# Performance work log

Hardware: AMD Instinct MI355X
Metric: run time of the kernel (lower is better)

## Reference

```python
import jax, jax.numpy as jnp
import numpy as np

B = 16      # number of point clouds
N = 4096    # points per cloud (max after densify)
D = 3       # xyz


def setup_inputs() -> dict:
    key = jax.random.key(0)
    k1, k2 = jax.random.split(key)
    pred = jax.random.normal(k1, (B * N, D), dtype=jnp.float32)
    target = jax.random.normal(k2, (B * N, D), dtype=jnp.float32)
    # sorted segment ids, equal-sized clouds (faithful to to_dense_batch usage)
    batch = jnp.repeat(jnp.arange(B, dtype=jnp.int64), N)
    return {"pred": pred, "target": target, "batch": batch}


def to_dense_batch(x, batch, num_batches, max_n):
    # PyG to_dense_batch: scatter flat points into [B, max_n, D], zero-padded.
    ones = jnp.ones_like(batch)
    counts = jax.ops.segment_sum(ones, batch, num_segments=num_batches)
    offsets = jnp.concatenate([jnp.zeros((1,), batch.dtype), jnp.cumsum(counts)[:-1]])
    pos = jnp.arange(batch.shape[0], dtype=batch.dtype) - offsets[batch]
    dense = jnp.zeros((num_batches, max_n, x.shape[-1]), x.dtype)
    return dense.at[batch, pos].set(x)


def chamfer_distance(x, y):
    # squared-euclidean pairwise distances via the GEMM identity
    x2 = jnp.sum(x * x, axis=-1)                      # [B, N]
    y2 = jnp.sum(y * y, axis=-1)                      # [B, M]
    xy = jnp.einsum('bnd,bmd->bnm', x, y)             # [B, N, M]
    d = x2[:, :, None] + y2[:, None, :] - 2.0 * xy    # [B, N, M]
    cham_x = jnp.mean(jnp.min(d, axis=2), axis=1)     # mean over N of min over M
    cham_y = jnp.mean(jnp.min(d, axis=1), axis=1)     # mean over M of min over N
    # point_reduction='mean', batch_reduction='mean' (pytorch3d defaults)
    return jnp.mean(cham_x + cham_y)


def reference(pred, target, batch):
    x = to_dense_batch(pred, batch, B, N)
    y = to_dense_batch(target, batch, B, N)
    return chamfer_distance(x, y)
```

## Files before the change

kernel.cpp:

```cpp
#include <hip/hip_runtime.h>


namespace {

constexpr int kB = 16;
constexpr int kN = 4096;
constexpr int kPlane = kB * kN;
constexpr int kJS = 4;
constexpr int kStage = 256;
constexpr int kNS = (kN / kJS) / kStage;
constexpr float kScale = 1.0f / (float)(kB * kN);

typedef short bf16x8 __attribute__((ext_vector_type(8)));
typedef float f32x4 __attribute__((ext_vector_type(4)));
typedef unsigned short u16;

__device__ inline u16 bf16_rn(float f) {
  union { float f; unsigned u; } v; v.f = f;
  unsigned r = v.u + 0x7fffu + ((v.u >> 16) & 1u);
  return (u16)(r >> 16);
}
__device__ inline float bf16_f(u16 h) {
  union { unsigned u; float f; } v; v.u = (unsigned)h << 16;
  return v.f;
}
__device__ inline unsigned pk2(u16 lo, u16 hi) {
  return (unsigned)lo | ((unsigned)hi << 16);
}

__global__ void init_out(float* out) { out[0] = 0.0f; }

__global__ __launch_bounds__(256) void cd_prep(
    const float* __restrict__ pred, const float* __restrict__ targ,
    u16* __restrict__ Apred, u16* __restrict__ Atarg,
    u16* __restrict__ Bpred, u16* __restrict__ Btarg,
    float* __restrict__ out) {
  const int p = blockIdx.x * 256 + threadIdx.x;
  if (p == 0) out[0] = 0.0f;
  const int cloud = p >> 12, q = p & (kN - 1);
  const int stg = q >> 8, pl = q & (kStage - 1);
  const size_t boff = (size_t)cloud * 65536 + (size_t)stg * 4096 + (size_t)pl * 8;
  const u16 one = 0x3F80;

  const float* srcs[2] = {pred, targ};
  u16* adsts[2] = {Apred, Atarg};
  u16* bdsts[2] = {Bpred, Btarg};
#pragma unroll
  for (int which = 0; which < 2; ++which) {
    const float a = srcs[which][3 * p], c = srcs[which][3 * p + 1],
                d = srcs[which][3 * p + 2];
    const u16 ah = bf16_rn(a), ch = bf16_rn(c), dh = bf16_rn(d);
    const u16 al = bf16_rn(a - bf16_f(ah));
    const u16 cl = bf16_rn(c - bf16_f(ch));
    const u16 dl = bf16_rn(d - bf16_f(dh));
    const float s2 = fmaf(a, a, fmaf(c, c, d * d));
    const u16 s2h = bf16_rn(s2);
    const u16 s2l = bf16_rn(s2 - bf16_f(s2h));
    {
      uint4 w0, w1;
      w0.x = pk2(ah, ch); w0.y = pk2(dh, al); w0.z = pk2(cl, dl); w0.w = pk2(ah, ch);
      w1.x = pk2(dh, al); w1.y = pk2(cl, dl); w1.z = pk2(s2h, s2l); w1.w = pk2(one, one);
      uint4* dst = reinterpret_cast<uint4*>(adsts[which] + (size_t)p * 16);
      dst[0] = w0; dst[1] = w1;
    }
    {
      const u16 nah = bf16_rn(-2.0f * bf16_f(ah));
      const u16 nch = bf16_rn(-2.0f * bf16_f(ch));
      const u16 ndh = bf16_rn(-2.0f * bf16_f(dh));
      const u16 nal = bf16_rn(-2.0f * bf16_f(al));
      const u16 ncl = bf16_rn(-2.0f * bf16_f(cl));
      const u16 ndl = bf16_rn(-2.0f * bf16_f(dl));
      uint4 w0, w1;
      w0.x = pk2(nah, nch); w0.y = pk2(ndh, nah); w0.z = pk2(nch, ndh); w0.w = pk2(nal, ncl);
      w1.x = pk2(ndl, nal); w1.y = pk2(ncl, ndl); w1.z = pk2(one, one); w1.w = pk2(s2h, s2l);
      *reinterpret_cast<uint4*>(bdsts[which] + boff) = w0;
      *reinterpret_cast<uint4*>(bdsts[which] + boff + 2048) = w1;
    }
  }
}

__global__ __launch_bounds__(256) void cd_mfma(
    const u16* __restrict__ Apred, const u16* __restrict__ Atarg,
    const u16* __restrict__ Bpred, const u16* __restrict__ Btarg,
    float* __restrict__ rowpart) {
  __shared__ uint4 Blds4[1028];

  const int t = threadIdx.x;
  const int w = t >> 6, lane = t & 63;
  const int l15 = lane & 15, kg = lane >> 4;
  const bool act = (kg < 2);
  const int g = kg & 1;
  const int bx = blockIdx.x;
  const int chunk = bx & 31;
  const int slice = bx >> 5;
  const int cloud = blockIdx.y;
  const int dir = blockIdx.z;
  const u16* __restrict__ A = dir ? Atarg : Apred;
  const u16* __restrict__ B = dir ? Bpred : Btarg;

  const int arow0 = cloud * kN + chunk * 128 + w * 32 + l15;
  union { uint4 u; bf16x8 v; } af0, af1;
  af0.u = make_uint4(0, 0, 0, 0);
  af1.u = make_uint4(0, 0, 0, 0);
  if (act) {
    af0.u = *reinterpret_cast<const uint4*>(A + (size_t)arow0 * 16 + g * 8);
    af1.u = *reinterpret_cast<const uint4*>(A + (size_t)(arow0 + 16) * 16 + g * 8);
  }

  const char* bsl = (const char*)B + (size_t)cloud * 131072 + (size_t)slice * 32768;
  char* ldsbase = (char*)Blds4;
#define STAGE(st, buf)                                                        \
  {                                                                           \
    const char* _src = bsl + (size_t)(st) * 8192;                             \
    char* _dst = ldsbase + (buf) * 8192;                                      \
    _Pragma("unroll")                                                         \
    for (int i = 0; i < 2; ++i) {                                             \
      __builtin_amdgcn_global_load_lds(                                       \
          (const __attribute__((address_space(1))) void*)(_src +              \
              ((w * 2 + i) * 64 + lane) * 16),                                \
          (__attribute__((address_space(3))) void*)(_dst + (w * 2 + i) * 1024),\
          16, 0, 0);                                                          \
    }                                                                         \
  }

  const int rb0 = act ? (g * 4096 + l15 * 16) : 16384;
  const int rstep = act ? 256 : 0;
  const int bufstep = act ? 8192 : 0;

  f32x4 z4;
#pragma unroll
  for (int r = 0; r < 4; ++r) z4[r] = 0.0f;
  float rmin0[4], rmin1[4];
#pragma unroll
  for (int r = 0; r < 4; ++r) { rmin0[r] = 1e30f; rmin1[r] = 1e30f; }

  STAGE(0, 0);
  if (t == 0) Blds4[1024] = make_uint4(0, 0, 0, 0);
  __syncthreads();

  for (int st = 0; st < kNS; ++st) {
    if (st < kNS - 1) STAGE(st + 1, (st + 1) & 1);
    const char* pb = ldsbase + rb0 + (st & 1) * bufstep;
#pragma unroll 4
    for (int jt = 0; jt < kStage / 16; ++jt) {
      union { uint4 u; bf16x8 v; } bu;
      bu.u = *reinterpret_cast<const uint4*>(pb);
      pb += rstep;
      const f32x4 s0 =
          __builtin_amdgcn_mfma_f32_16x16x32_bf16(af0.v, bu.v, z4, 0, 0, 0);
      const f32x4 s1 =
          __builtin_amdgcn_mfma_f32_16x16x32_bf16(af1.v, bu.v, z4, 0, 0, 0);
#pragma unroll
      for (int r = 0; r < 4; ++r) {
        rmin0[r] = fminf(rmin0[r], s0[r]);
        rmin1[r] = fminf(rmin1[r], s1[r]);
      }
    }
    __syncthreads();
  }
#undef STAGE

#pragma unroll
  for (int sh = 1; sh < 16; sh <<= 1) {
#pragma unroll
    for (int r = 0; r < 4; ++r) {
      rmin0[r] = fminf(rmin0[r], __shfl_xor(rmin0[r], sh, 64));
      rmin1[r] = fminf(rmin1[r], __shfl_xor(rmin1[r], sh, 64));
    }
  }
  if (l15 == 0) {
    float* rp = rowpart + (((size_t)dir * kJS + slice) * kB + cloud) * kN +
                chunk * 128 + w * 32;
#pragma unroll
    for (int r = 0; r < 4; ++r) {
      rp[kg * 4 + r] = rmin0[r];
      rp[16 + kg * 4 + r] = rmin1[r];
    }
  }
}

__global__ __launch_bounds__(256) void cd_reduce(
    const float* __restrict__ rowpart, float* __restrict__ out) {
  const int u = blockIdx.x * 256 + threadIdx.x;
  const int dir = u >> 16, rest = u & 65535;
  const int cloud = rest >> 12, row = rest & (kN - 1);
  float rm = 1e30f;
#pragma unroll
  for (int s2 = 0; s2 < kJS; ++s2)
    rm = fminf(rm, rowpart[(((size_t)dir * kJS + s2) * kB + cloud) * kN + row]);
  float s = rm;
  for (int o = 32; o > 0; o >>= 1) s += __shfl_down(s, o, 64);
  __shared__ float wsum[4];
  const int lane = threadIdx.x & 63, wv = threadIdx.x >> 6;
  if (lane == 0) wsum[wv] = s;
  __syncthreads();
  if (threadIdx.x == 0)
    atomicAdd(out, (wsum[0] + wsum[1] + wsum[2] + wsum[3]) * kScale);
}

template <int KX>
__global__ __launch_bounds__(256) void chamfer_direct(
    const float* __restrict__ pred, const float* __restrict__ targ,
    float* __restrict__ out) {
  __shared__ float4 tA[128], tB[128];
  const int t = threadIdx.x;
  const int xb = blockIdx.x, b = blockIdx.y, dir = blockIdx.z;
  const float* __restrict__ X = dir ? targ : pred;
  const float* __restrict__ Y = dir ? pred : targ;
  float2 xx2[KX], xy2[KX], xz2[KX];
  float x2[KX], mn[KX];
  const int ibase = b * kN + xb * (256 * KX) + t;
#pragma unroll
  for (int k = 0; k < KX; ++k) {
    const int i = ibase + k * 256;
    const float a = X[3 * i], c = X[3 * i + 1], d = X[3 * i + 2];
    x2[k] = fmaf(a, a, fmaf(c, c, d * d));
    xx2[k] = make_float2(-2.0f * a, -2.0f * a);
    xy2[k] = make_float2(-2.0f * c, -2.0f * c);
    xz2[k] = make_float2(-2.0f * d, -2.0f * d);
    mn[k] = 1e30f;
  }
  for (int t0 = 0; t0 < kN; t0 += 256) {
    __syncthreads();
    if (t < 128) {
      const int j0 = 3 * (b * kN + t0 + 2 * t);
      const float a0 = Y[j0], c0 = Y[j0 + 1], d0 = Y[j0 + 2];
      const float a1 = Y[j0 + 3], c1 = Y[j0 + 4], d1 = Y[j0 + 5];
      tA[t] = make_float4(a0, a1, c0, c1);
      tB[t] = make_float4(d0, d1, fmaf(a0, a0, fmaf(c0, c0, d0 * d0)),
                          fmaf(a1, a1, fmaf(c1, c1, d1 * d1)));
    }
    __syncthreads();
    for (int jj = 0; jj < 128; ++jj) {
      const float4 qa = tA[jj], qb = tB[jj];
      const float2 qx = make_float2(qa.x, qa.y), qy = make_float2(qa.z, qa.w);
      const float2 qz = make_float2(qb.x, qb.y), qw = make_float2(qb.z, qb.w);
#pragma unroll
      for (int k = 0; k < KX; ++k) {
        float2 acc;
        asm("v_pk_fma_f32 %0, %1, %2, %3\n\t"
            "v_pk_fma_f32 %0, %4, %5, %0\n\t"
            "v_pk_fma_f32 %0, %6, %7, %0"
            : "=&v"(acc)
            : "v"(xz2[k]), "v"(qz), "v"(qw), "v"(xy2[k]), "v"(qy),
              "v"(xx2[k]), "v"(qx));
        asm("v_min3_f32 %0, %0, %1, %2" : "+v"(mn[k]) : "v"(acc.x), "v"(acc.y));
      }
    }
  }
  float s = 0.0f;
#pragma unroll
  for (int k = 0; k < KX; ++k) s += x2[k] + mn[k];
  for (int o = 32; o > 0; o >>= 1) s += __shfl_down(s, o, 64);
  __shared__ float wsum[4];
  const int lane = t & 63, wv = t >> 6;
  if (lane == 0) wsum[wv] = s;
  __syncthreads();
  if (t == 0)
    atomicAdd(out, (wsum[0] + wsum[1] + wsum[2] + wsum[3]) * kScale);
}

}

extern "C" void kernel_launch(void* const* d_in, const int* in_sizes, int n_in,
                              void* d_out, int out_size, void* d_ws,
                              size_t ws_size, hipStream_t stream) {
  const float* pred = (const float*)d_in[0];
  const float* targ = (const float*)d_in[1];
  float* out = (float*)d_out;

  const size_t needOne = (size_t)kPlane * 16 * sizeof(u16);
  const size_t needRow = (size_t)2 * kJS * kPlane * sizeof(float) / kB * kB;
  const size_t needRowB = (size_t)2 * kJS * kB * kN * sizeof(float);
  (void)needRow;
  if (ws_size >= 4 * needOne + needRowB) {
    u16* Apred = (u16*)d_ws;
    u16* Atarg = (u16*)((char*)d_ws + needOne);
    u16* Bpred = (u16*)((char*)d_ws + 2 * needOne);
    u16* Btarg = (u16*)((char*)d_ws + 3 * needOne);
    float* rowpart = (float*)((char*)d_ws + 4 * needOne);
    cd_prep<<<dim3(kPlane / 256), 256, 0, stream>>>(pred, targ, Apred, Atarg,
                                                    Bpred, Btarg, out);
    cd_mfma<<<dim3(32 * kJS, kB, 2), 256, 0, stream>>>(Apred, Atarg, Bpred,
                                                       Btarg, rowpart);
    cd_reduce<<<dim3(2 * kPlane / 256), 256, 0, stream>>>(rowpart, out);
  } else {
    init_out<<<dim3(1), dim3(1), 0, stream>>>(out);
    constexpr int KX = 8;
    dim3 grid(kN / (256 * KX), kB, 2);
    chamfer_direct<KX><<<grid, 256, 0, stream>>>(pred, targ, out);
  }
}
```

Measured before the change: 106.4 us.

## Switch distance MFMA to 32x32x16 bf16 with min3 reduction and fewer slices

Replaces the 16x16x32 MFMA tiles, where half the lanes were idle and fed zero operands, with 32x32x16 MFMA tiles that use all 64 lanes. The A/B packed layouts are reordered to match the new K-split across lane halves. Per-row minima are folded with v_min3 across two MFMA results, and the column-slice count drops from 4 to 2, so each block handles more columns and the reduce pass reads fewer partials. The costs are a larger accumulator register footprint per wave and half as many blocks, which lowers parallelism.

```diff
diff --git a/kernel.cpp b/kernel.cpp
--- a/kernel.cpp
+++ b/kernel.cpp
@@ -6,13 +6,13 @@
 constexpr int kB = 16;
 constexpr int kN = 4096;
 constexpr int kPlane = kB * kN;
-constexpr int kJS = 4;
+constexpr int kJS = 2;
 constexpr int kStage = 256;
 constexpr int kNS = (kN / kJS) / kStage;
 constexpr float kScale = 1.0f / (float)(kB * kN);
 
 typedef short bf16x8 __attribute__((ext_vector_type(8)));
-typedef float f32x4 __attribute__((ext_vector_type(4)));
+typedef float f32x16 __attribute__((ext_vector_type(16)));
 typedef unsigned short u16;
 
 __device__ inline u16 bf16_rn(float f) {
@@ -59,7 +59,7 @@
     {
       uint4 w0, w1;
       w0.x = pk2(ah, ch); w0.y = pk2(dh, al); w0.z = pk2(cl, dl); w0.w = pk2(ah, ch);
-      w1.x = pk2(dh, al); w1.y = pk2(cl, dl); w1.z = pk2(s2h, s2l); w1.w = pk2(one, one);
+      w1.x = pk2(dh, s2h); w1.y = pk2(s2l, one); w1.z = pk2(one, al); w1.w = pk2(cl, dl);
       uint4* dst = reinterpret_cast<uint4*>(adsts[which] + (size_t)p * 16);
       dst[0] = w0; dst[1] = w1;
     }
@@ -72,7 +72,7 @@
       const u16 ndl = bf16_rn(-2.0f * bf16_f(dl));
       uint4 w0, w1;
       w0.x = pk2(nah, nch); w0.y = pk2(ndh, nah); w0.z = pk2(nch, ndh); w0.w = pk2(nal, ncl);
-      w1.x = pk2(ndl, nal); w1.y = pk2(ncl, ndl); w1.z = pk2(one, one); w1.w = pk2(s2h, s2l);
+      w1.x = pk2(ndl, one); w1.y = pk2(one, s2h); w1.z = pk2(s2l, nal); w1.w = pk2(ncl, ndl);
       *reinterpret_cast<uint4*>(bdsts[which] + boff) = w0;
       *reinterpret_cast<uint4*>(bdsts[which] + boff + 2048) = w1;
     }
@@ -83,13 +83,11 @@
     const u16* __restrict__ Apred, const u16* __restrict__ Atarg,
     const u16* __restrict__ Bpred, const u16* __restrict__ Btarg,
     float* __restrict__ rowpart) {
-  __shared__ uint4 Blds4[1028];
+  __shared__ uint4 Blds4[1024];
 
   const int t = threadIdx.x;
   const int w = t >> 6, lane = t & 63;
-  const int l15 = lane & 15, kg = lane >> 4;
-  const bool act = (kg < 2);
-  const int g = kg & 1;
+  const int half = lane >> 5, l31 = lane & 31;
   const int bx = blockIdx.x;
   const int chunk = bx & 31;
   const int slice = bx >> 5;
@@ -98,16 +96,13 @@
   const u16* __restrict__ A = dir ? Atarg : Apred;
   const u16* __restrict__ B = dir ? Bpred : Btarg;
 
-  const int arow0 = cloud * kN + chunk * 128 + w * 32 + l15;
-  union { uint4 u; bf16x8 v; } af0, af1;
-  af0.u = make_uint4(0, 0, 0, 0);
-  af1.u = make_uint4(0, 0, 0, 0);
-  if (act) {
-    af0.u = *reinterpret_cast<const uint4*>(A + (size_t)arow0 * 16 + g * 8);
-    af1.u = *reinterpret_cast<const uint4*>(A + (size_t)(arow0 + 16) * 16 + g * 8);
-  }
-
-  const char* bsl = (const char*)B + (size_t)cloud * 131072 + (size_t)slice * 32768;
+  const int arow = cloud * kN + chunk * 128 + w * 32 + l31;
+  union U { uint4 u; bf16x8 v; };
+  U af;
+  af.u = *reinterpret_cast<const uint4*>(A + (size_t)arow * 16 + half * 8);
+
+  const char* bsl = (const char*)B + (size_t)cloud * 131072 +
+                    (size_t)slice * 65536;
   char* ldsbase = (char*)Blds4;
 #define STAGE(st, buf)                                                        \
   {                                                                           \
@@ -123,58 +118,50 @@
     }                                                                         \
   }
 
-  const int rb0 = act ? (g * 4096 + l15 * 16) : 16384;
-  const int rstep = act ? 256 : 0;
-  const int bufstep = act ? 8192 : 0;
-
-  f32x4 z4;
-#pragma unroll
-  for (int r = 0; r < 4; ++r) z4[r] = 0.0f;
-  float rmin0[4], rmin1[4];
-#pragma unroll
-  for (int r = 0; r < 4; ++r) { rmin0[r] = 1e30f; rmin1[r] = 1e30f; }
+  f32x16 zacc;
+#pragma unroll
+  for (int r = 0; r < 16; ++r) zacc[r] = 0.0f;
+  float rmin[16];
+#pragma unroll
+  for (int r = 0; r < 16; ++r) rmin[r] = 1e30f;
 
   STAGE(0, 0);
-  if (t == 0) Blds4[1024] = make_uint4(0, 0, 0, 0);
   __syncthreads();
 
   for (int st = 0; st < kNS; ++st) {
     if (st < kNS - 1) STAGE(st + 1, (st + 1) & 1);
-    const char* pb = ldsbase + rb0 + (st & 1) * bufstep;
-#pragma unroll 4
-    for (int jt = 0; jt < kStage / 16; ++jt) {
-      union { uint4 u; bf16x8 v; } bu;
-      bu.u = *reinterpret_cast<const uint4*>(pb);
-      pb += rstep;
-      const f32x4 s0 =
-          __builtin_amdgcn_mfma_f32_16x16x32_bf16(af0.v, bu.v, z4, 0, 0, 0);
-      const f32x4 s1 =
-          __builtin_amdgcn_mfma_f32_16x16x32_bf16(af1.v, bu.v, z4, 0, 0, 0);
-#pragma unroll
-      for (int r = 0; r < 4; ++r) {
-        rmin0[r] = fminf(rmin0[r], s0[r]);
-        rmin1[r] = fminf(rmin1[r], s1[r]);
-      }
+    const char* hb = ldsbase + (st & 1) * 8192 + half * 4096 + l31 * 16;
+#pragma unroll
+    for (int jt = 0; jt < kStage / 64; ++jt) {
+      U b0, b1;
+      b0.u = *reinterpret_cast<const uint4*>(hb + jt * 1024);
+      b1.u = *reinterpret_cast<const uint4*>(hb + jt * 1024 + 512);
+      const f32x16 s0 =
+          __builtin_amdgcn_mfma_f32_32x32x16_bf16(af.v, b0.v, zacc, 0, 0, 0);
+      const f32x16 s1 =
+          __builtin_amdgcn_mfma_f32_32x32x16_bf16(af.v, b1.v, zacc, 0, 0, 0);
+#pragma unroll
+      for (int r = 0; r < 16; ++r)
+        asm("v_min3_f32 %0, %0, %1, %2"
+            : "+v"(rmin[r]) : "v"(s0[r]), "v"(s1[r]));
     }
     __syncthreads();
   }
 #undef STAGE
 
 #pragma unroll
-  for (int sh = 1; sh < 16; sh <<= 1) {
-#pragma unroll
-    for (int r = 0; r < 4; ++r) {
-      rmin0[r] = fminf(rmin0[r], __shfl_xor(rmin0[r], sh, 64));
-      rmin1[r] = fminf(rmin1[r], __shfl_xor(rmin1[r], sh, 64));
-    }
-  }
-  if (l15 == 0) {
+  for (int sh = 1; sh < 32; sh <<= 1) {
+#pragma unroll
+    for (int r = 0; r < 16; ++r)
+      rmin[r] = fminf(rmin[r], __shfl_xor(rmin[r], sh, 64));
+  }
+  if (l31 == 0) {
     float* rp = rowpart + (((size_t)dir * kJS + slice) * kB + cloud) * kN +
                 chunk * 128 + w * 32;
 #pragma unroll
-    for (int r = 0; r < 4; ++r) {
-      rp[kg * 4 + r] = rmin0[r];
-      rp[16 + kg * 4 + r] = rmin1[r];
+    for (int r = 0; r < 16; ++r) {
+      const int row = (r & 3) + 8 * (r >> 2) + 4 * half;
+      rp[row] = rmin[r];
     }
   }
 }
@@ -270,10 +257,8 @@
   float* out = (float*)d_out;
 
   const size_t needOne = (size_t)kPlane * 16 * sizeof(u16);
-  const size_t needRow = (size_t)2 * kJS * kPlane * sizeof(float) / kB * kB;
-  const size_t needRowB = (size_t)2 * kJS * kB * kN * sizeof(float);
-  (void)needRow;
-  if (ws_size >= 4 * needOne + needRowB) {
+  const size_t needRow = (size_t)2 * kJS * kB * kN * sizeof(float);
+  if (ws_size >= 4 * needOne + needRow) {
     u16* Apred = (u16*)d_ws;
     u16* Atarg = (u16*)((char*)d_ws + needOne);
     u16* Bpred = (u16*)((char*)d_ws + 2 * needOne);
```

Measured after the change: 99.79 us. 6.2% less time.
